# Kernel tuning notes

Measured on AMD Instinct MI355X. Metric: run time of the kernel, lower is better.

## Reference

```python
import jax, jax.numpy as jnp
import numpy as np
from jax.ops import segment_sum, segment_max, segment_min

B_, T_, V_, H_, W_ = 1, 8, 6, 96, 160
NUM_TRACKS = 512          # track ids in [-1, NUM_TRACKS)
THR = 2.0                 # distance_threshold
DKS = 0.05                # duplicate_keep_scale
NEG = -1e30


def setup_inputs() -> dict:
    key = jax.random.key(0)
    ks = jax.random.split(key, 10)
    shp = (B_, T_, V_, H_, W_)
    f = lambda k, c: jax.random.normal(k, shp + (c,), jnp.float32)
    return {
        "center": f(ks[0], 3),
        "offset": f(ks[1], 3),
        "opacity": f(ks[2], 1),
        "scale": f(ks[3], 3),
        "rotation": f(ks[4], 4),
        "feat_dc": f(ks[5], 3),
        "keep_score": f(ks[6], 1),
        "instance_affinity": f(ks[7], 32),
        "motion_code": f(ks[8], 16),
        "global_track_id": jax.random.randint(ks[9], shp, -1, NUM_TRACKS),
    }


def _merge(floats, gid):
    center, offset, opacity, scale, rotation, feat_dc, keep, inst, motion = floats
    b, t, v, h, w = gid.shape
    B, N = b * t, v * h * w
    BN = B * N
    S = B * NUM_TRACKS            # one segment per (frame, track id); S = dummy segment
    nseg = S + 1

    ids = gid.reshape(BN)
    bt = jnp.arange(BN) // N
    valid = ids >= 0
    seg = jnp.where(valid, bt * NUM_TRACKS + jnp.maximum(ids, 0), S)

    # tracks with >= 2 cells participate (torch: mask.sum() < 2 -> skip)
    cnt = segment_sum(valid.astype(jnp.int32), seg, num_segments=nseg)
    dup = valid & (cnt[seg] >= 2)
    seg1 = jnp.where(dup, seg, S)

    flat = lambda x: x.reshape(BN, x.shape[-1])
    k0 = flat(keep)[:, 0]
    c = flat(center)

    def seg_softmax(mask, sgm):
        # numerically stable segment softmax of k0 restricted to mask
        m = segment_max(jnp.where(mask, k0, NEG), sgm, num_segments=nseg)
        arg = jnp.where(mask, k0 - m[sgm], 0.0)   # keep grads finite on masked lanes
        e = jnp.where(mask, jnp.exp(arg), 0.0)
        z = segment_sum(e, sgm, num_segments=nseg)
        return e / jnp.maximum(z[sgm], 1e-20), m

    # pass 1: softmax-weighted mean center over all cells of the track
    w1, _ = seg_softmax(dup, seg1)
    mc1 = segment_sum(w1[:, None] * c, seg1, num_segments=nseg)
    dist = jnp.linalg.norm(c - mc1[seg1], axis=-1)
    active = dup & (dist <= THR)

    # pass 2: softmax restricted to active cells
    seg2 = jnp.where(active, seg, S)
    w2, m2 = seg_softmax(active, seg2)

    # representative = argmax weight (== argmax keep score), first occurrence on ties
    idx = jnp.arange(BN)
    cand = jnp.where(active & (k0 == m2[seg2]), idx, BN)
    rep = segment_min(cand, seg2, num_segments=nseg)
    is_rep = active & (idx == rep[seg2])

    def wmean(x):
        xf = flat(x)
        return segment_sum(w2[:, None] * xf, seg2, num_segments=nseg)[seg2]

    mcen = wmean(center)
    moff = wmean(offset)
    mop = wmean(opacity)
    msc = wmean(scale)
    mrot_seg = segment_sum(w2[:, None] * flat(rotation), seg2, num_segments=nseg)
    mrot_seg = mrot_seg / jnp.maximum(
        jnp.linalg.norm(mrot_seg, axis=-1, keepdims=True), 1e-12)  # F.normalize
    mrot = mrot_seg[seg2]
    mfd = wmean(feat_dc)
    minst = wmean(inst)
    mmot = wmean(motion)
    kf = flat(keep)
    mkeep = segment_max(jnp.where(active[:, None], kf, NEG), seg2,
                        num_segments=nseg)[seg2]

    a = active[:, None]
    sfac = jnp.where(is_rep, 1.0, DKS)[:, None]   # duplicates suppressed
    out = jnp.concatenate([
        jnp.where(a, mcen, c),
        jnp.where(a, moff, flat(offset)),
        jnp.where(a, mop * sfac, flat(opacity)),
        jnp.where(a, msc, flat(scale)),
        jnp.where(a, mrot, flat(rotation)),
        jnp.where(a, mfd, flat(feat_dc)),
        jnp.where(a, mkeep * sfac, kf),
        jnp.where(a, minst, flat(inst)),
        jnp.where(a, mmot, flat(motion)),
    ], axis=-1)
    return out.reshape(b, t, v, h, w, -1)


def reference(center, offset, opacity, scale, rotation, feat_dc, keep_score,
              instance_affinity, motion_code, global_track_id):
    floats = (center, offset, opacity, scale, rotation, feat_dc, keep_score,
              instance_affinity, motion_code)
    return _merge(floats, global_track_id)
```

## Files before the change

### kernel.cpp

```cpp
#include <hip/hip_runtime.h>

static constexpr int kBN   = 737280;
static constexpr int kSlab = 92160;
static constexpr int kNT   = 512;
static constexpr int kNSeg = 4096;
static constexpr int kChunk = 5120;

__global__ __launch_bounds__(1024) void k_count(const int* __restrict__ gid, int* cnt) {
    __shared__ int h[kNT];
    int tid = threadIdx.x;
    if (tid < kNT) h[tid] = 0;
    __syncthreads();
    int chunk0 = blockIdx.x * kChunk;
    int bt = chunk0 / kSlab;
    for (int j = tid; j < kChunk; j += 1024) {
        int id = gid[chunk0 + j];
        if (id >= 0) atomicAdd(&h[id], 1);
    }
    __syncthreads();
    if (tid < kNT) { int v = h[tid]; if (v) atomicAdd(&cnt[bt * kNT + tid], v); }
}

__global__ __launch_bounds__(1024) void k_scan(const int* __restrict__ cnt, int* offs, int* cursor) {
    __shared__ int part[1024];
    int tid = threadIdx.x;
    int b = tid * 4;
    int v0 = cnt[b], v1 = cnt[b + 1], v2 = cnt[b + 2], v3 = cnt[b + 3];
    int s01 = v0 + v1, s = s01 + v2 + v3;
    part[tid] = s;
    __syncthreads();
    for (int off = 1; off < 1024; off <<= 1) {
        int t = (tid >= off) ? part[tid - off] : 0;
        __syncthreads();
        part[tid] += t;
        __syncthreads();
    }
    int base = part[tid] - s;
    int o0 = base, o1 = base + v0, o2 = base + s01, o3 = base + s01 + v2;
    offs[b] = o0; offs[b + 1] = o1; offs[b + 2] = o2; offs[b + 3] = o3;
    cursor[b] = o0; cursor[b + 1] = o1; cursor[b + 2] = o2; cursor[b + 3] = o3;
}

__global__ __launch_bounds__(1024) void k_fill(const int* __restrict__ gid, int* cursor, int* lists) {
    __shared__ int lcnt[kNT];
    __shared__ int lbase[kNT];
    int tid = threadIdx.x;
    if (tid < kNT) lcnt[tid] = 0;
    __syncthreads();
    int chunk0 = blockIdx.x * kChunk;
    int bt = chunk0 / kSlab;
    int rank[5], ids[5];
#pragma unroll
    for (int u = 0; u < 5; u++) {
        int id = gid[chunk0 + tid + u * 1024];
        ids[u] = id;
        rank[u] = (id >= 0) ? atomicAdd(&lcnt[id], 1) : 0;
    }
    __syncthreads();
    if (tid < kNT) { int c = lcnt[tid]; lbase[tid] = c ? atomicAdd(&cursor[bt * kNT + tid], c) : 0; }
    __syncthreads();
#pragma unroll
    for (int u = 0; u < 5; u++) {
        int id = ids[u];
        if (id >= 0) lists[lbase[id] + rank[u]] = chunk0 + tid + u * 1024;
    }
}

template<int CNT>
__device__ __forceinline__ void wreduce_store(float (&a)[17], int lane, int tb, float* totl) {
#pragma unroll
    for (int c = 0; c < CNT; c++) {
        float v = a[c];
#pragma unroll
        for (int m = 1; m < 64; m <<= 1) v += __shfl_xor(v, m, 64);
        if (lane == 0) totl[tb + c] = v;
    }
}

__global__ __launch_bounds__(256, 4) void k_seg(
        const int* __restrict__ lists, const int* __restrict__ offs, const int* __restrict__ cnt,
        const float* __restrict__ keep, const float* __restrict__ center,
        const float* __restrict__ offsetp, const float* __restrict__ opacity,
        const float* __restrict__ scale, const float* __restrict__ rot,
        const float* __restrict__ fd, const float* __restrict__ inst,
        const float* __restrict__ motion,
        float* __restrict__ mc1g, int* __restrict__ repg,
        float* __restrict__ merged) {
    int s = ((blockIdx.x & 7) << 9) | (blockIdx.x >> 3);
    int n = cnt[s];
    if (n < 2) return;
    int base = offs[s];
    int tid = threadIdx.x;
    int lane = tid & 63;
    int wv = tid >> 6;

    __shared__ int   idxs[256];
    __shared__ float kk[256];
    __shared__ float c0s[256], c1s[256], c2s[256];
    __shared__ float e2s[256];
    __shared__ float red4[256][5];
    __shared__ float wm1[4], wm2[4];
    __shared__ int   wri[4];
    __shared__ float totl[66];

    float lmax = -1e30f;
    for (int j = tid; j < n; j += 256) {
        int i = lists[base + j];
        float k = keep[i];
        float cx = center[3 * i + 0], cy = center[3 * i + 1], cz = center[3 * i + 2];
        if (j < 256) { idxs[j] = i; kk[j] = k; c0s[j] = cx; c1s[j] = cy; c2s[j] = cz; }
        lmax = fmaxf(lmax, k);
    }
#pragma unroll
    for (int m = 1; m < 64; m <<= 1) lmax = fmaxf(lmax, __shfl_xor(lmax, m, 64));
    if (lane == 0) wm1[wv] = lmax;
    __syncthreads();
    float m1 = fmaxf(fmaxf(wm1[0], wm1[1]), fmaxf(wm1[2], wm1[3]));

    float lz = 0.f, l0 = 0.f, l1 = 0.f, l2 = 0.f;
    for (int j = tid; j < n; j += 256) {
        float k, cx, cy, cz;
        if (j < 256) { k = kk[j]; cx = c0s[j]; cy = c1s[j]; cz = c2s[j]; }
        else { int i = lists[base + j]; k = keep[i];
               cx = center[3 * i + 0]; cy = center[3 * i + 1]; cz = center[3 * i + 2]; }
        float e = expf(k - m1);
        lz += e; l0 += e * cx; l1 += e * cy; l2 += e * cz;
    }
    red4[tid][0] = lz; red4[tid][1] = l0; red4[tid][2] = l1; red4[tid][3] = l2;
    __syncthreads();
    for (int o = 128; o; o >>= 1) {
        if (tid < o) {
            red4[tid][0] += red4[tid + o][0]; red4[tid][1] += red4[tid + o][1];
            red4[tid][2] += red4[tid + o][2]; red4[tid][3] += red4[tid + o][3];
        }
        __syncthreads();
    }
    float z1 = red4[0][0];
    float inv1 = 1.0f / fmaxf(z1, 1e-20f);
    float mc0 = red4[0][1] * inv1, mcy = red4[0][2] * inv1, mcz = red4[0][3] * inv1;

    float lm2 = -1e30f;
    for (int j = tid; j < n; j += 256) {
        float k, cx, cy, cz;
        if (j < 256) { k = kk[j]; cx = c0s[j]; cy = c1s[j]; cz = c2s[j]; }
        else { int i = lists[base + j]; k = keep[i];
               cx = center[3 * i + 0]; cy = center[3 * i + 1]; cz = center[3 * i + 2]; }
        float d0 = cx - mc0, d1 = cy - mcy, d2 = cz - mcz;
        bool act = sqrtf(d0 * d0 + d1 * d1 + d2 * d2) <= 2.0f;
        if (j < 256) e2s[j] = act ? 1.0f : 0.0f;
        if (act) lm2 = fmaxf(lm2, k);
    }
#pragma unroll
    for (int m = 1; m < 64; m <<= 1) lm2 = fmaxf(lm2, __shfl_xor(lm2, m, 64));
    if (lane == 0) wm2[wv] = lm2;
    __syncthreads();
    float m2 = fmaxf(fmaxf(wm2[0], wm2[1]), fmaxf(wm2[2], wm2[3]));

    int lrep = 0x7fffffff;
    for (int j = tid; j < n; j += 256) {
        if (j < 256) {
            bool act = e2s[j] != 0.0f;
            float k = kk[j];
            float e = act ? expf(k - m2) : 0.0f;
            e2s[j] = e;
            if (act && k == m2) lrep = min(lrep, idxs[j]);
        } else {
            int i = lists[base + j];
            float k = keep[i];
            float cx = center[3 * i + 0], cy = center[3 * i + 1], cz = center[3 * i + 2];
            float d0 = cx - mc0, d1 = cy - mcy, d2 = cz - mcz;
            if (sqrtf(d0 * d0 + d1 * d1 + d2 * d2) <= 2.0f && k == m2) lrep = min(lrep, i);
        }
    }
#pragma unroll
    for (int m = 1; m < 64; m <<= 1) lrep = min(lrep, __shfl_xor(lrep, m, 64));
    if (lane == 0) wri[wv] = lrep;
    __syncthreads();
    int rep = min(min(wri[0], wri[1]), min(wri[2], wri[3]));

    {
        float a[17];
#pragma unroll
        for (int c = 0; c < 17; c++) a[c] = 0.f;

        auto e2_glob = [&](int j, int& i) -> float {
            i = lists[base + j];
            float k = keep[i];
            float cx = center[3 * i + 0], cy = center[3 * i + 1], cz = center[3 * i + 2];
            float d0 = cx - mc0, d1 = cy - mcy, d2 = cz - mcz;
            return (sqrtf(d0 * d0 + d1 * d1 + d2 * d2) <= 2.0f) ? expf(k - m2) : 0.0f;
        };

        if (wv == 0) {
            for (int j = lane; j < n; j += 64) {
                float e, cx, cy, cz; int i;
                if (j < 256) { e = e2s[j]; i = idxs[j]; cx = c0s[j]; cy = c1s[j]; cz = c2s[j]; }
                else { e = e2_glob(j, i);
                       cx = center[3 * i + 0]; cy = center[3 * i + 1]; cz = center[3 * i + 2]; }
                if (e != 0.0f) {
                    a[0] += e * cx; a[1] += e * cy; a[2] += e * cz;
                    a[3] += e * offsetp[3 * i + 0]; a[4] += e * offsetp[3 * i + 1]; a[5] += e * offsetp[3 * i + 2];
                    a[6] += e * opacity[i];
                    a[7] += e * scale[3 * i + 0]; a[8] += e * scale[3 * i + 1]; a[9] += e * scale[3 * i + 2];
                    float4 r4 = *(const float4*)(rot + 4 * i);
                    a[10] += e * r4.x; a[11] += e * r4.y; a[12] += e * r4.z; a[13] += e * r4.w;
                    a[14] += e * fd[3 * i + 0]; a[15] += e * fd[3 * i + 1]; a[16] += e * fd[3 * i + 2];
                }
            }
            wreduce_store<17>(a, lane, 0, totl);
        } else if (wv == 1) {
            for (int j = lane; j < n; j += 64) {
                float e; int i;
                if (j < 256) { e = e2s[j]; i = idxs[j]; } else { e = e2_glob(j, i); }
                if (e != 0.0f) {
                    const float4* ip = (const float4*)(inst + 32 * i);
#pragma unroll
                    for (int q = 0; q < 4; q++) {
                        float4 v = ip[q];
                        a[4 * q + 0] += e * v.x; a[4 * q + 1] += e * v.y;
                        a[4 * q + 2] += e * v.z; a[4 * q + 3] += e * v.w;
                    }
                }
            }
            wreduce_store<16>(a, lane, 17, totl);
        } else if (wv == 2) {
            for (int j = lane; j < n; j += 64) {
                float e; int i;
                if (j < 256) { e = e2s[j]; i = idxs[j]; } else { e = e2_glob(j, i); }
                if (e != 0.0f) {
                    const float4* ip = (const float4*)(inst + 32 * i) + 4;
#pragma unroll
                    for (int q = 0; q < 4; q++) {
                        float4 v = ip[q];
                        a[4 * q + 0] += e * v.x; a[4 * q + 1] += e * v.y;
                        a[4 * q + 2] += e * v.z; a[4 * q + 3] += e * v.w;
                    }
                }
            }
            wreduce_store<16>(a, lane, 33, totl);
        } else {
            for (int j = lane; j < n; j += 64) {
                float e; int i;
                if (j < 256) { e = e2s[j]; i = idxs[j]; } else { e = e2_glob(j, i); }
                if (e != 0.0f) {
                    const float4* mp = (const float4*)(motion + 16 * i);
#pragma unroll
                    for (int q = 0; q < 4; q++) {
                        float4 v = mp[q];
                        a[4 * q + 0] += e * v.x; a[4 * q + 1] += e * v.y;
                        a[4 * q + 2] += e * v.z; a[4 * q + 3] += e * v.w;
                    }
                    a[16] += e;
                }
            }
            wreduce_store<17>(a, lane, 49, totl);
        }
    }
    __syncthreads();

    if (tid < 66) {
        float z2v = totl[65];
        float inv2 = 1.0f / fmaxf(z2v, 1e-20f);
        float v;
        if (tid < 10) v = totl[tid] * inv2;
        else if (tid < 14) {
            float q0 = totl[10] * inv2, q1 = totl[11] * inv2;
            float q2 = totl[12] * inv2, q3 = totl[13] * inv2;
            float nrm = sqrtf(q0 * q0 + q1 * q1 + q2 * q2 + q3 * q3);
            float rn = 1.0f / fmaxf(nrm, 1e-12f);
            v = (totl[tid] * inv2) * rn;
        }
        else if (tid < 17) v = totl[tid] * inv2;
        else if (tid == 17) v = m2;
        else v = totl[tid - 1] * inv2;
        merged[(long)s * 66 + tid] = v;
    }
    if (tid == 0) {
        mc1g[3 * s + 0] = mc0; mc1g[3 * s + 1] = mcy; mc1g[3 * s + 2] = mcz;
        repg[s] = rep;
    }
}

__global__ __launch_bounds__(256) void k_out(
        const int* __restrict__ gid, const int* __restrict__ cnt,
        const float* __restrict__ keep, const float* __restrict__ center,
        const float* __restrict__ offsetp, const float* __restrict__ opacity,
        const float* __restrict__ scale, const float* __restrict__ rot,
        const float* __restrict__ fd, const float* __restrict__ inst,
        const float* __restrict__ motion,
        const float* __restrict__ mc1g, const int* __restrict__ repg,
        const float* __restrict__ merged,
        float* __restrict__ out) {
    __shared__ float rec[64][68];
    __shared__ int   asg[64];
    __shared__ float sf[64];
    int tid = threadIdx.x;
    int e0 = blockIdx.x * 64;

    if (tid < 192) {
        rec[tid / 3][0  + tid % 3] = center [e0 * 3 + tid];
        rec[tid / 3][3  + tid % 3] = offsetp[e0 * 3 + tid];
        rec[tid / 3][7  + tid % 3] = scale  [e0 * 3 + tid];
        rec[tid / 3][14 + tid % 3] = fd     [e0 * 3 + tid];
    }
    if (tid < 64) {
        rec[tid][6]  = opacity[e0 + tid];
        rec[tid][17] = keep   [e0 + tid];
    }
    rec[tid >> 2][10 + (tid & 3)] = rot[e0 * 4 + tid];
    for (int f = tid; f < 2048; f += 256) rec[f >> 5][18 + (f & 31)] = inst  [e0 * 32 + f];
    for (int f = tid; f < 1024; f += 256) rec[f >> 4][50 + (f & 15)] = motion[e0 * 16 + f];
    __syncthreads();

    if (tid < 64) {
        int e = e0 + tid;
        int id = gid[e];
        int sg = -1; float sv = 1.0f;
        if (id >= 0) {
            int seg = (e / kSlab) * kNT + id;
            if (cnt[seg] >= 2) {
                float d0 = rec[tid][0] - mc1g[3 * seg + 0];
                float d1 = rec[tid][1] - mc1g[3 * seg + 1];
                float d2 = rec[tid][2] - mc1g[3 * seg + 2];
                if (sqrtf(d0 * d0 + d1 * d1 + d2 * d2) <= 2.0f) {
                    sg = seg;
                    sv = (e == repg[seg]) ? 1.0f : 0.05f;
                }
            }
        }
        asg[tid] = sg; sf[tid] = sv;
    }
    __syncthreads();

    for (int f = tid; f < 64 * 66; f += 256) {
        int elem = f / 66;
        int sg = asg[elem];
        if (sg >= 0) {
            int c = f - elem * 66;
            float v = merged[(long)sg * 66 + c];
            if (c == 6 || c == 17) v *= sf[elem];
            rec[elem][c] = v;
        }
    }
    __syncthreads();

    float2* o2 = reinterpret_cast<float2*>(out + (size_t)e0 * 66);
    for (int f = tid; f < 64 * 33; f += 256) {
        int elem = f / 33;
        int c2 = f - elem * 33;
        o2[f] = *(const float2*)&rec[elem][c2 * 2];
    }
}

extern "C" void kernel_launch(void* const* d_in, const int* in_sizes, int n_in,
                              void* d_out, int out_size, void* d_ws, size_t ws_size,
                              hipStream_t stream) {
    const float* center = (const float*)d_in[0];
    const float* offsetp = (const float*)d_in[1];
    const float* opacity = (const float*)d_in[2];
    const float* scale = (const float*)d_in[3];
    const float* rot = (const float*)d_in[4];
    const float* fd = (const float*)d_in[5];
    const float* keep = (const float*)d_in[6];
    const float* inst = (const float*)d_in[7];
    const float* motion = (const float*)d_in[8];
    const int* gid = (const int*)d_in[9];
    float* out = (float*)d_out;

    int* cnt      = (int*)d_ws;
    int* offs     = (int*)d_ws + 4096;
    int* cursor   = (int*)d_ws + 8192;
    float* mc1g   = (float*)d_ws + 12288;
    int* repg     = (int*)d_ws + 28672;
    float* merged = (float*)d_ws + 32768;
    int* lists    = (int*)d_ws + 303104;

    hipMemsetAsync(cnt, 0, (size_t)kNSeg * 4, stream);

    k_count<<<kBN / kChunk, 1024, 0, stream>>>(gid, cnt);
    k_scan<<<1, 1024, 0, stream>>>(cnt, offs, cursor);
    k_fill<<<kBN / kChunk, 1024, 0, stream>>>(gid, cursor, lists);
    k_seg<<<kNSeg, 256, 0, stream>>>(lists, offs, cnt, keep, center, offsetp, opacity,
                                     scale, rot, fd, inst, motion, mc1g, repg, merged);
    k_out<<<kBN / 64, 256, 0, stream>>>(gid, cnt, keep, center, offsetp, opacity, scale,
                                        rot, fd, inst, motion, mc1g, repg, merged, out);
}
```

Baseline: 465.7 us.

## Write merged outputs directly from segment kernel and copy only non-duplicate cells

The segment kernel now scatters final output rows itself. Active cells get the merged record, with opacity and keep scaled for non-representatives, and inactive duplicates get a passthrough copy using values it already loads. The old output kernel, which re-read every input plus the per-segment merged buffers, is replaced by a simple copy kernel that exits early for cells in duplicate tracks. This removes the intermediate merged, mc1g and repg round-trip and a re-read of all inputs for duplicate cells, but the scattered 66-float row writes from the segment kernel are uncoalesced and k_rest writes scalars per thread with a stride of 66.

New measurement: 476.1 us. 1.02x slower.

```diff
diff --git a/kernel.cpp b/kernel.cpp
--- a/kernel.cpp
+++ b/kernel.cpp
@@ -84,8 +84,7 @@
         const float* __restrict__ scale, const float* __restrict__ rot,
         const float* __restrict__ fd, const float* __restrict__ inst,
         const float* __restrict__ motion,
-        float* __restrict__ mc1g, int* __restrict__ repg,
-        float* __restrict__ merged) {
+        float* __restrict__ out) {
     int s = ((blockIdx.x & 7) << 9) | (blockIdx.x >> 3);
     int n = cnt[s];
     if (n < 2) return;
@@ -102,6 +101,7 @@
     __shared__ float wm1[4], wm2[4];
     __shared__ int   wri[4];
     __shared__ float totl[66];
+    __shared__ float mrec[66];
 
     float lmax = -1e30f;
     for (int j = tid; j < n; j += 256) {
@@ -178,33 +178,47 @@
     __syncthreads();
     int rep = min(min(wri[0], wri[1]), min(wri[2], wri[3]));
 
+    auto e2_glob = [&](int j, int& i) -> float {
+        i = lists[base + j];
+        float k = keep[i];
+        float d0 = center[3 * i + 0] - mc0;
+        float d1 = center[3 * i + 1] - mcy;
+        float d2 = center[3 * i + 2] - mcz;
+        return (sqrtf(d0 * d0 + d1 * d1 + d2 * d2) <= 2.0f) ? expf(k - m2) : 0.0f;
+    };
+
     {
         float a[17];
 #pragma unroll
         for (int c = 0; c < 17; c++) a[c] = 0.f;
 
-        auto e2_glob = [&](int j, int& i) -> float {
-            i = lists[base + j];
-            float k = keep[i];
-            float cx = center[3 * i + 0], cy = center[3 * i + 1], cz = center[3 * i + 2];
-            float d0 = cx - mc0, d1 = cy - mcy, d2 = cz - mcz;
-            return (sqrtf(d0 * d0 + d1 * d1 + d2 * d2) <= 2.0f) ? expf(k - m2) : 0.0f;
-        };
-
         if (wv == 0) {
             for (int j = lane; j < n; j += 64) {
-                float e, cx, cy, cz; int i;
-                if (j < 256) { e = e2s[j]; i = idxs[j]; cx = c0s[j]; cy = c1s[j]; cz = c2s[j]; }
-                else { e = e2_glob(j, i);
+                float e, cx, cy, cz, k; int i;
+                if (j < 256) { e = e2s[j]; i = idxs[j]; cx = c0s[j]; cy = c1s[j]; cz = c2s[j]; k = kk[j]; }
+                else { e = e2_glob(j, i); k = keep[i];
                        cx = center[3 * i + 0]; cy = center[3 * i + 1]; cz = center[3 * i + 2]; }
+                float o0 = offsetp[3 * i + 0], o1 = offsetp[3 * i + 1], o2 = offsetp[3 * i + 2];
+                float op = opacity[i];
+                float s0 = scale[3 * i + 0], s1 = scale[3 * i + 1], s2 = scale[3 * i + 2];
+                float4 r4 = *(const float4*)(rot + 4 * i);
+                float f0 = fd[3 * i + 0], f1 = fd[3 * i + 1], f2 = fd[3 * i + 2];
                 if (e != 0.0f) {
                     a[0] += e * cx; a[1] += e * cy; a[2] += e * cz;
-                    a[3] += e * offsetp[3 * i + 0]; a[4] += e * offsetp[3 * i + 1]; a[5] += e * offsetp[3 * i + 2];
-                    a[6] += e * opacity[i];
-                    a[7] += e * scale[3 * i + 0]; a[8] += e * scale[3 * i + 1]; a[9] += e * scale[3 * i + 2];
-                    float4 r4 = *(const float4*)(rot + 4 * i);
+                    a[3] += e * o0; a[4] += e * o1; a[5] += e * o2;
+                    a[6] += e * op;
+                    a[7] += e * s0; a[8] += e * s1; a[9] += e * s2;
                     a[10] += e * r4.x; a[11] += e * r4.y; a[12] += e * r4.z; a[13] += e * r4.w;
-                    a[14] += e * fd[3 * i + 0]; a[15] += e * fd[3 * i + 1]; a[16] += e * fd[3 * i + 2];
+                    a[14] += e * f0; a[15] += e * f1; a[16] += e * f2;
+                } else {
+                    float* o = out + (long)66 * i;
+                    o[0] = cx; o[1] = cy; o[2] = cz;
+                    o[3] = o0; o[4] = o1; o[5] = o2;
+                    o[6] = op;
+                    o[7] = s0; o[8] = s1; o[9] = s2;
+                    o[10] = r4.x; o[11] = r4.y; o[12] = r4.z; o[13] = r4.w;
+                    o[14] = f0; o[15] = f1; o[16] = f2;
+                    o[17] = k;
                 }
             }
             wreduce_store<17>(a, lane, 0, totl);
@@ -212,14 +226,19 @@
             for (int j = lane; j < n; j += 64) {
                 float e; int i;
                 if (j < 256) { e = e2s[j]; i = idxs[j]; } else { e = e2_glob(j, i); }
+                const float4* ip = (const float4*)(inst + 32 * i);
+                float4 v0 = ip[0], v1 = ip[1], v2 = ip[2], v3 = ip[3];
                 if (e != 0.0f) {
-                    const float4* ip = (const float4*)(inst + 32 * i);
-#pragma unroll
-                    for (int q = 0; q < 4; q++) {
-                        float4 v = ip[q];
-                        a[4 * q + 0] += e * v.x; a[4 * q + 1] += e * v.y;
-                        a[4 * q + 2] += e * v.z; a[4 * q + 3] += e * v.w;
-                    }
+                    a[0]  += e * v0.x; a[1]  += e * v0.y; a[2]  += e * v0.z; a[3]  += e * v0.w;
+                    a[4]  += e * v1.x; a[5]  += e * v1.y; a[6]  += e * v1.z; a[7]  += e * v1.w;
+                    a[8]  += e * v2.x; a[9]  += e * v2.y; a[10] += e * v2.z; a[11] += e * v2.w;
+                    a[12] += e * v3.x; a[13] += e * v3.y; a[14] += e * v3.z; a[15] += e * v3.w;
+                } else {
+                    float2* o = (float2*)(out + (long)66 * i + 18);
+                    o[0] = make_float2(v0.x, v0.y); o[1] = make_float2(v0.z, v0.w);
+                    o[2] = make_float2(v1.x, v1.y); o[3] = make_float2(v1.z, v1.w);
+                    o[4] = make_float2(v2.x, v2.y); o[5] = make_float2(v2.z, v2.w);
+                    o[6] = make_float2(v3.x, v3.y); o[7] = make_float2(v3.z, v3.w);
                 }
             }
             wreduce_store<16>(a, lane, 17, totl);
@@ -227,14 +246,19 @@
             for (int j = lane; j < n; j += 64) {
                 float e; int i;
                 if (j < 256) { e = e2s[j]; i = idxs[j]; } else { e = e2_glob(j, i); }
+                const float4* ip = (const float4*)(inst + 32 * i) + 4;
+                float4 v0 = ip[0], v1 = ip[1], v2 = ip[2], v3 = ip[3];
                 if (e != 0.0f) {
-                    const float4* ip = (const float4*)(inst + 32 * i) + 4;
-#pragma unroll
-                    for (int q = 0; q < 4; q++) {
-                        float4 v = ip[q];
-                        a[4 * q + 0] += e * v.x; a[4 * q + 1] += e * v.y;
-                        a[4 * q + 2] += e * v.z; a[4 * q + 3] += e * v.w;
-                    }
+                    a[0]  += e * v0.x; a[1]  += e * v0.y; a[2]  += e * v0.z; a[3]  += e * v0.w;
+                    a[4]  += e * v1.x; a[5]  += e * v1.y; a[6]  += e * v1.z; a[7]  += e * v1.w;
+                    a[8]  += e * v2.x; a[9]  += e * v2.y; a[10] += e * v2.z; a[11] += e * v2.w;
+                    a[12] += e * v3.x; a[13] += e * v3.y; a[14] += e * v3.z; a[15] += e * v3.w;
+                } else {
+                    float2* o = (float2*)(out + (long)66 * i + 34);
+                    o[0] = make_float2(v0.x, v0.y); o[1] = make_float2(v0.z, v0.w);
+                    o[2] = make_float2(v1.x, v1.y); o[3] = make_float2(v1.z, v1.w);
+                    o[4] = make_float2(v2.x, v2.y); o[5] = make_float2(v2.z, v2.w);
+                    o[6] = make_float2(v3.x, v3.y); o[7] = make_float2(v3.z, v3.w);
                 }
             }
             wreduce_store<16>(a, lane, 33, totl);
@@ -242,15 +266,20 @@
             for (int j = lane; j < n; j += 64) {
                 float e; int i;
                 if (j < 256) { e = e2s[j]; i = idxs[j]; } else { e = e2_glob(j, i); }
+                const float4* mp = (const float4*)(motion + 16 * i);
+                float4 v0 = mp[0], v1 = mp[1], v2 = mp[2], v3 = mp[3];
                 if (e != 0.0f) {
-                    const float4* mp = (const float4*)(motion + 16 * i);
-#pragma unroll
-                    for (int q = 0; q < 4; q++) {
-                        float4 v = mp[q];
-                        a[4 * q + 0] += e * v.x; a[4 * q + 1] += e * v.y;
-                        a[4 * q + 2] += e * v.z; a[4 * q + 3] += e * v.w;
-                    }
+                    a[0]  += e * v0.x; a[1]  += e * v0.y; a[2]  += e * v0.z; a[3]  += e * v0.w;
+                    a[4]  += e * v1.x; a[5]  += e * v1.y; a[6]  += e * v1.z; a[7]  += e * v1.w;
+                    a[8]  += e * v2.x; a[9]  += e * v2.y; a[10] += e * v2.z; a[11] += e * v2.w;
+                    a[12] += e * v3.x; a[13] += e * v3.y; a[14] += e * v3.z; a[15] += e * v3.w;
                     a[16] += e;
+                } else {
+                    float2* o = (float2*)(out + (long)66 * i + 50);
+                    o[0] = make_float2(v0.x, v0.y); o[1] = make_float2(v0.z, v0.w);
+                    o[2] = make_float2(v1.x, v1.y); o[3] = make_float2(v1.z, v1.w);
+                    o[4] = make_float2(v2.x, v2.y); o[5] = make_float2(v2.z, v2.w);
+                    o[6] = make_float2(v3.x, v3.y); o[7] = make_float2(v3.z, v3.w);
                 }
             }
             wreduce_store<17>(a, lane, 49, totl);
@@ -273,82 +302,63 @@
         else if (tid < 17) v = totl[tid] * inv2;
         else if (tid == 17) v = m2;
         else v = totl[tid - 1] * inv2;
-        merged[(long)s * 66 + tid] = v;
-    }
-    if (tid == 0) {
-        mc1g[3 * s + 0] = mc0; mc1g[3 * s + 1] = mcy; mc1g[3 * s + 2] = mcz;
-        repg[s] = rep;
-    }
-}
-
-__global__ __launch_bounds__(256) void k_out(
+        mrec[tid] = v;
+    }
+    __syncthreads();
+
+    for (int f = tid; f < n * 33; f += 256) {
+        int j = f / 33;
+        int c2 = f - 33 * j;
+        int i; bool act;
+        if (j < 256) { act = e2s[j] != 0.0f; i = idxs[j]; }
+        else { float e = e2_glob(j, i); act = e != 0.0f; }
+        if (act) {
+            float2 v = make_float2(mrec[2 * c2], mrec[2 * c2 + 1]);
+            if (i != rep) {
+                if (c2 == 3) v.x *= 0.05f;
+                else if (c2 == 8) v.y *= 0.05f;
+            }
+            *(float2*)(out + (long)66 * i + 2 * c2) = v;
+        }
+    }
+}
+
+__global__ __launch_bounds__(256) void k_rest(
         const int* __restrict__ gid, const int* __restrict__ cnt,
         const float* __restrict__ keep, const float* __restrict__ center,
         const float* __restrict__ offsetp, const float* __restrict__ opacity,
         const float* __restrict__ scale, const float* __restrict__ rot,
         const float* __restrict__ fd, const float* __restrict__ inst,
         const float* __restrict__ motion,
-        const float* __restrict__ mc1g, const int* __restrict__ repg,
-        const float* __restrict__ merged,
         float* __restrict__ out) {
-    __shared__ float rec[64][68];
-    __shared__ int   asg[64];
-    __shared__ float sf[64];
-    int tid = threadIdx.x;
-    int e0 = blockIdx.x * 64;
-
-    if (tid < 192) {
-        rec[tid / 3][0  + tid % 3] = center [e0 * 3 + tid];
-        rec[tid / 3][3  + tid % 3] = offsetp[e0 * 3 + tid];
-        rec[tid / 3][7  + tid % 3] = scale  [e0 * 3 + tid];
-        rec[tid / 3][14 + tid % 3] = fd     [e0 * 3 + tid];
-    }
-    if (tid < 64) {
-        rec[tid][6]  = opacity[e0 + tid];
-        rec[tid][17] = keep   [e0 + tid];
-    }
-    rec[tid >> 2][10 + (tid & 3)] = rot[e0 * 4 + tid];
-    for (int f = tid; f < 2048; f += 256) rec[f >> 5][18 + (f & 31)] = inst  [e0 * 32 + f];
-    for (int f = tid; f < 1024; f += 256) rec[f >> 4][50 + (f & 15)] = motion[e0 * 16 + f];
-    __syncthreads();
-
-    if (tid < 64) {
-        int e = e0 + tid;
-        int id = gid[e];
-        int sg = -1; float sv = 1.0f;
-        if (id >= 0) {
-            int seg = (e / kSlab) * kNT + id;
-            if (cnt[seg] >= 2) {
-                float d0 = rec[tid][0] - mc1g[3 * seg + 0];
-                float d1 = rec[tid][1] - mc1g[3 * seg + 1];
-                float d2 = rec[tid][2] - mc1g[3 * seg + 2];
-                if (sqrtf(d0 * d0 + d1 * d1 + d2 * d2) <= 2.0f) {
-                    sg = seg;
-                    sv = (e == repg[seg]) ? 1.0f : 0.05f;
-                }
-            }
-        }
-        asg[tid] = sg; sf[tid] = sv;
-    }
-    __syncthreads();
-
-    for (int f = tid; f < 64 * 66; f += 256) {
-        int elem = f / 66;
-        int sg = asg[elem];
-        if (sg >= 0) {
-            int c = f - elem * 66;
-            float v = merged[(long)sg * 66 + c];
-            if (c == 6 || c == 17) v *= sf[elem];
-            rec[elem][c] = v;
-        }
-    }
-    __syncthreads();
-
-    float2* o2 = reinterpret_cast<float2*>(out + (size_t)e0 * 66);
-    for (int f = tid; f < 64 * 33; f += 256) {
-        int elem = f / 33;
-        int c2 = f - elem * 33;
-        o2[f] = *(const float2*)&rec[elem][c2 * 2];
+    int i = blockIdx.x * 256 + threadIdx.x;
+    int id = gid[i];
+    if (id >= 0 && cnt[(i / kSlab) * kNT + id] >= 2) return;
+    float* o = out + (long)i * 66;
+    o[0] = center[3 * i + 0]; o[1] = center[3 * i + 1]; o[2] = center[3 * i + 2];
+#pragma unroll
+    for (int c = 0; c < 3; c++) o[3 + c] = offsetp[3 * i + c];
+    o[6] = opacity[i];
+#pragma unroll
+    for (int c = 0; c < 3; c++) o[7 + c] = scale[3 * i + c];
+    float4 r4 = *(const float4*)(rot + 4 * i);
+    o[10] = r4.x; o[11] = r4.y; o[12] = r4.z; o[13] = r4.w;
+#pragma unroll
+    for (int c = 0; c < 3; c++) o[14 + c] = fd[3 * i + c];
+    o[17] = keep[i];
+    const float4* ip = (const float4*)(inst + 32 * i);
+#pragma unroll
+    for (int q = 0; q < 8; q++) {
+        float4 v = ip[q];
+        o[18 + 4 * q + 0] = v.x; o[18 + 4 * q + 1] = v.y;
+        o[18 + 4 * q + 2] = v.z; o[18 + 4 * q + 3] = v.w;
+    }
+    const float4* mp = (const float4*)(motion + 16 * i);
+#pragma unroll
+    for (int q = 0; q < 4; q++) {
+        float4 v = mp[q];
+        o[50 + 4 * q + 0] = v.x; o[50 + 4 * q + 1] = v.y;
+        o[50 + 4 * q + 2] = v.z; o[50 + 4 * q + 3] = v.w;
     }
 }
 
@@ -367,13 +377,10 @@
     const int* gid = (const int*)d_in[9];
     float* out = (float*)d_out;
 
-    int* cnt      = (int*)d_ws;
-    int* offs     = (int*)d_ws + 4096;
-    int* cursor   = (int*)d_ws + 8192;
-    float* mc1g   = (float*)d_ws + 12288;
-    int* repg     = (int*)d_ws + 28672;
-    float* merged = (float*)d_ws + 32768;
-    int* lists    = (int*)d_ws + 303104;
+    int* cnt    = (int*)d_ws;
+    int* offs   = (int*)d_ws + 4096;
+    int* cursor = (int*)d_ws + 8192;
+    int* lists  = (int*)d_ws + 12288;
 
     hipMemsetAsync(cnt, 0, (size_t)kNSeg * 4, stream);
 
@@ -381,7 +388,7 @@
     k_scan<<<1, 1024, 0, stream>>>(cnt, offs, cursor);
     k_fill<<<kBN / kChunk, 1024, 0, stream>>>(gid, cursor, lists);
     k_seg<<<kNSeg, 256, 0, stream>>>(lists, offs, cnt, keep, center, offsetp, opacity,
-                                     scale, rot, fd, inst, motion, mc1g, repg, merged);
-    k_out<<<kBN / 64, 256, 0, stream>>>(gid, cnt, keep, center, offsetp, opacity, scale,
-                                        rot, fd, inst, motion, mc1g, repg, merged, out);
-}
+                                     scale, rot, fd, inst, motion, out);
+    k_rest<<<kBN / 256, 256, 0, stream>>>(gid, cnt, keep, center, offsetp, opacity, scale,
+                                          rot, fd, inst, motion, out);
+}
```
